# Kernel tuning notes

Measured on AMD Instinct MI355X. Metric: run time of the kernel, lower is better.

## Reference

```python
import jax, jax.numpy as jnp
import numpy as np

N = 1024                      # FFT length (init kwarg)
NF = N // 2 + 1               # rfft output length = len(freq)
PB_LO = 40.0 / 60.0           # pulse_band[0] in Hz
PB_HI = 180.0 / 60.0          # pulse_band[1] in Hz
DELTA_HZ = 6.0 / 60.0         # self.delta after /60
W0, W1 = 1.0, 1.0             # weights[0], weights[1]
B, T = 32768, 1024


def setup_inputs() -> dict:
    key = jax.random.key(0)
    k1, k2 = jax.random.split(key)
    preds = jax.random.normal(k1, (B, T), dtype=jnp.float32)
    # realistic camera frame rates ~25-35 Hz (must exceed 2*pulse_band[1]=6 Hz)
    Fs = 25.0 + 10.0 * jax.random.uniform(k2, (B,), dtype=jnp.float32)
    return {"preds": preds, "Fs": Fs}


def reference(preds, Fs):
    idx = jnp.arange(NF)                                            # [Nf]
    # freq = linspace(0, Fs/2, Nf) per sample -> [B, Nf]
    freq = (Fs[:, None] * 0.5) * (idx.astype(jnp.float32) / (NF - 1))
    left = jnp.argmin(jnp.abs(freq - PB_LO), axis=1)                # [B] int
    right = jnp.argmin(jnp.abs(freq - PB_HI), axis=1)               # [B] int

    psd = jnp.abs(jnp.fft.rfft(preds, n=N)) ** 2                    # [B, Nf]
    total = jnp.sum(psd, axis=-1)                                   # [B]

    l = left[:, None]
    r = right[:, None]
    out_band = (idx < l) | (idx >= r)                               # psd[:left] + psd[right:]
    band_loss = jnp.sum(jnp.where(out_band, psd, 0.0), axis=-1) / (1e-8 + total)

    in_band = (idx >= l) & (idx < r)
    # argmax(psd[left:right]) + left  (psd >= 0, so -inf mask is safe)
    peak = jnp.argmax(jnp.where(in_band, psd, -jnp.inf), axis=1)    # [B]
    # delta = max(1, round(self.delta / (Fs/2/len(freq))))  (round half-to-even, as Python)
    delta = jnp.maximum(1.0, jnp.round(DELTA_HZ / (Fs * 0.5 / NF))).astype(jnp.int32)

    p = peak[:, None]
    d = delta[:, None]
    # psd[left:peak-delta] + psd[peak+delta:right]  (empty slices -> 0 via mask)
    sparse_mask = in_band & ((idx < p - d) | (idx >= p + d))
    num = jnp.sum(jnp.where(sparse_mask, psd, 0.0), axis=-1)
    # sum(psd[left:right] + 1e-8) adds 1e-8 per in-band bin, keep faithful
    den = jnp.sum(jnp.where(in_band, psd + 1e-8, 0.0), axis=-1)
    sparse_loss = num / den

    return W0 * jnp.mean(band_loss) + W1 * jnp.mean(sparse_loss)
```

## Files before the change

kernel.cpp:

```cpp
#include <hip/hip_runtime.h>
#include <cmath>

#define BATCH 32768
#define SROW 66

struct cplx { float x, y; };
__device__ __forceinline__ cplx cadd(cplx a, cplx b){ return {a.x+b.x, a.y+b.y}; }
__device__ __forceinline__ cplx csub(cplx a, cplx b){ return {a.x-b.x, a.y-b.y}; }
__device__ __forceinline__ cplx cmul(cplx a, cplx b){ return {a.x*b.x - a.y*b.y, a.x*b.y + a.y*b.x}; }
__device__ __forceinline__ cplx cmul_mi(cplx a){ return {a.y, -a.x}; }
__device__ __forceinline__ cplx cmul_w81(cplx a){ const float c=0.70710678f; return {c*(a.x+a.y), c*(a.y-a.x)}; }
__device__ __forceinline__ cplx cmul_w83(cplx a){ const float c=0.70710678f; return {c*(a.y-a.x), -c*(a.x+a.y)}; }

__device__ __forceinline__ void dft8(cplx a[8]) {
    cplx t0=cadd(a[0],a[4]), t4=csub(a[0],a[4]);
    cplx t1=cadd(a[1],a[5]), t5=csub(a[1],a[5]);
    cplx t2=cadd(a[2],a[6]), t6=csub(a[2],a[6]);
    cplx t3=cadd(a[3],a[7]), t7=csub(a[3],a[7]);
    cplx u0=cadd(t0,t2), u2=csub(t0,t2);
    cplx u1=cadd(t1,t3), u3=cmul_mi(csub(t1,t3));
    a[0]=cadd(u0,u1); a[4]=csub(u0,u1); a[2]=cadd(u2,u3); a[6]=csub(u2,u3);
    cplx v0=t4, v1=cmul_w81(t5), v2=cmul_mi(t6), v3=cmul_w83(t7);
    cplx w0=cadd(v0,v2), w2=csub(v0,v2);
    cplx w1=cadd(v1,v3), w3=cmul_mi(csub(v1,v3));
    a[1]=cadd(w0,w1); a[5]=csub(w0,w1); a[3]=cadd(w2,w3); a[7]=csub(w2,w3);
}

__device__ __forceinline__ int nearest_bin(float fs, float target) {
    float x = target * 1024.0f / fs;
    int i0 = (int)floorf(x);
    int lo = max(0, i0 - 1), hi = min(512, i0 + 2);
    int bi = lo; float bd = 1e30f;
    for (int i = lo; i <= hi; ++i) {
        float fr = (fs * 0.5f) * ((float)i / 512.0f);
        float d = fabsf(fr - target);
        if (d < bd) { bd = d; bi = i; }
    }
    return bi;
}

__global__ __launch_bounds__(256) void fft_loss_kernel(
    const float* __restrict__ preds, const float* __restrict__ Fs,
    float* __restrict__ blockpartial)
{
    __shared__ float2 lds[4][8 * SROW];
    __shared__ float sblk[4];

    const int tid  = threadIdx.x;
    const int wv   = tid >> 6;
    const int lane = tid & 63;
    const int row  = blockIdx.x * 4 + wv;

    float2* sm = lds[wv];
    const float2* x2 = reinterpret_cast<const float2*>(preds) + (size_t)row * 512;

    cplx z[8];
#pragma unroll
    for (int n1 = 0; n1 < 8; ++n1) {
        float2 v = x2[n1 * 64 + lane];
        z[n1] = {v.x, v.y};
    }
    dft8(z);
    {
        float sb, cb;
        __sincosf(-0.012271846f * (float)lane, &sb, &cb);
        cplx w = {cb, sb}, u = w;
#pragma unroll
        for (int r = 1; r < 8; ++r) { z[r] = cmul(z[r], u); u = cmul(u, w); }
    }
#pragma unroll
    for (int r = 0; r < 8; ++r) sm[r * SROW + lane] = make_float2(z[r].x, z[r].y);

    const int rB = lane & 7, m0 = lane >> 3;
    cplx b[8];
#pragma unroll
    for (int m1 = 0; m1 < 8; ++m1) {
        float2 v = sm[rB * SROW + 8 * m1 + m0];
        b[m1] = {v.x, v.y};
    }
    dft8(b);
    {
        float sb, cb;
        __sincosf(-0.09817477f * (float)m0, &sb, &cb);
        cplx w = {cb, sb}, u = w;
#pragma unroll
        for (int s = 1; s < 8; ++s) { b[s] = cmul(b[s], u); u = cmul(u, w); }
    }
#pragma unroll
    for (int s = 0; s < 8; ++s) {
        sm[rB * SROW + 8 * m0 + ((s + m0) & 7)] = make_float2(b[s].x, b[s].y);
    }

    const int sC = lane >> 3;
    cplx c[8];
#pragma unroll
    for (int m = 0; m < 8; ++m) {
        float2 v = sm[rB * SROW + 8 * m + ((sC + m) & 7)];
        c[m] = {v.x, v.y};
    }
    dft8(c);

    const float fs  = Fs[row];
    const int left  = nearest_bin(fs, (float)(40.0 / 60.0));
    const int right = nearest_bin(fs, 3.0f);
    const int pl    = (64 - lane) & 63;

    float psd[8];
    float total = 0.f, inb = 0.f, best = -1.f;
    int besti = 1 << 30;
    float sk, ck;
    __sincosf(-0.0061359233f * (float)lane, &sk, &ck);
    cplx wk = {ck, sk};
    const cplx wstep = {0.92387953f, -0.38268343f};
#pragma unroll
    for (int t = 0; t < 8; ++t) {
        cplx a = c[t];
        float px = __shfl(c[7 - t].x, pl);
        float py = __shfl(c[7 - t].y, pl);
        if (lane == 0) { px = c[(8 - t) & 7].x; py = c[(8 - t) & 7].y; }
        float ex = 0.5f * (a.x + px), ey = 0.5f * (a.y - py);
        float dx = a.x - px,          dy = a.y + py;
        float ox = 0.5f * dy,         oy = -0.5f * dx;
        float Xr = ex + wk.x * ox - wk.y * oy;
        float Xi = ey + wk.x * oy + wk.y * ox;
        float v  = Xr * Xr + Xi * Xi;
        psd[t] = v;
        total += v;
        int k = lane + 64 * t;
        if (k >= left && k < right) {
            inb += v;
            if (v > best) { best = v; besti = k; }
        }
        wk = cmul(wk, wstep);
    }
    if (lane == 0) {
        float d = c[0].x - c[0].y;
        total += d * d;
    }

#pragma unroll
    for (int off = 32; off > 0; off >>= 1) {
        total += __shfl_down(total, off);
        inb   += __shfl_down(inb, off);
        float ob = __shfl_down(best, off);
        int   oi = __shfl_down(besti, off);
        if (ob > best || (ob == best && oi < besti)) { best = ob; besti = oi; }
    }
    const int bbi = __shfl(besti, 0);
    int delta = (int)rintf(0.1f / ((fs * 0.5f) / 513.0f));
    if (delta < 1) delta = 1;
    const int lo = max(left, bbi - delta), hi = min(right, bbi + delta);
    float wsum = 0.f;
#pragma unroll
    for (int t = 0; t < 8; ++t) {
        int k = lane + 64 * t;
        if (k >= lo && k < hi) wsum += psd[t];
    }
#pragma unroll
    for (int off = 32; off > 0; off >>= 1) wsum += __shfl_down(wsum, off);

    if (lane == 0) {
        float band = (total - inb) / (1e-8f + total);
        float den  = inb + 1e-8f * (float)(right - left);
        sblk[wv] = band + (inb - wsum) / den;
    }
    __syncthreads();
    if (tid == 0) blockpartial[blockIdx.x] = sblk[0] + sblk[1] + sblk[2] + sblk[3];
}

__global__ __launch_bounds__(1024) void reduce_kernel(
    const float* __restrict__ bp, float* __restrict__ out)
{
    __shared__ float w[16];
    const int t = threadIdx.x;
    float acc = 0.f;
#pragma unroll
    for (int i = 0; i < 8; ++i) acc += bp[t + 1024 * i];
    for (int off = 32; off > 0; off >>= 1) acc += __shfl_down(acc, off);
    const int lane = t & 63, wvi = t >> 6;
    if (lane == 0) w[wvi] = acc;
    __syncthreads();
    if (t == 0) {
        float s = 0.f;
        for (int i = 0; i < 16; ++i) s += w[i];
        out[0] = s * (1.0f / (float)BATCH);
    }
}

extern "C" void kernel_launch(void* const* d_in, const int* in_sizes, int n_in,
                              void* d_out, int out_size, void* d_ws, size_t ws_size,
                              hipStream_t stream) {
    const float* preds = (const float*)d_in[0];
    const float* Fs    = (const float*)d_in[1];
    float* bp          = (float*)d_ws;
    float* out         = (float*)d_out;

    fft_loss_kernel<<<BATCH / 4, 256, 0, stream>>>(preds, Fs, bp);
    reduce_kernel<<<1, 1024, 0, stream>>>(bp, out);
}
```

Baseline: 194.5 us.

## Process two rows per wave with vectorized complex math and DPP reductions

```diff
diff --git a/kernel.cpp b/kernel.cpp
--- a/kernel.cpp
+++ b/kernel.cpp
@@ -2,28 +2,50 @@
 #include <cmath>
 
 #define BATCH 32768
-#define SROW 66
-
-struct cplx { float x, y; };
-__device__ __forceinline__ cplx cadd(cplx a, cplx b){ return {a.x+b.x, a.y+b.y}; }
-__device__ __forceinline__ cplx csub(cplx a, cplx b){ return {a.x-b.x, a.y-b.y}; }
-__device__ __forceinline__ cplx cmul(cplx a, cplx b){ return {a.x*b.x - a.y*b.y, a.x*b.y + a.y*b.x}; }
-__device__ __forceinline__ cplx cmul_mi(cplx a){ return {a.y, -a.x}; }
-__device__ __forceinline__ cplx cmul_w81(cplx a){ const float c=0.70710678f; return {c*(a.x+a.y), c*(a.y-a.x)}; }
-__device__ __forceinline__ cplx cmul_w83(cplx a){ const float c=0.70710678f; return {c*(a.y-a.x), -c*(a.x+a.y)}; }
-
-__device__ __forceinline__ void dft8(cplx a[8]) {
-    cplx t0=cadd(a[0],a[4]), t4=csub(a[0],a[4]);
-    cplx t1=cadd(a[1],a[5]), t5=csub(a[1],a[5]);
-    cplx t2=cadd(a[2],a[6]), t6=csub(a[2],a[6]);
-    cplx t3=cadd(a[3],a[7]), t7=csub(a[3],a[7]);
-    cplx u0=cadd(t0,t2), u2=csub(t0,t2);
-    cplx u1=cadd(t1,t3), u3=cmul_mi(csub(t1,t3));
-    a[0]=cadd(u0,u1); a[4]=csub(u0,u1); a[2]=cadd(u2,u3); a[6]=csub(u2,u3);
-    cplx v0=t4, v1=cmul_w81(t5), v2=cmul_mi(t6), v3=cmul_w83(t7);
-    cplx w0=cadd(v0,v2), w2=csub(v0,v2);
-    cplx w1=cadd(v1,v3), w3=cmul_mi(csub(v1,v3));
-    a[1]=cadd(w0,w1); a[5]=csub(w0,w1); a[3]=cadd(w2,w3); a[7]=csub(w2,w3);
+#define SROW  66
+
+typedef float v2f __attribute__((ext_vector_type(2)));
+
+__device__ __forceinline__ v2f mkc(float r, float i) { v2f t; t.x = r; t.y = i; return t; }
+__device__ __forceinline__ v2f cmul(v2f a, v2f b) {
+    v2f s = mkc(-a.y, a.x);
+    return a * b.x + s * b.y;
+}
+__device__ __forceinline__ v2f cmul_mi(v2f a){ return mkc(a.y, -a.x); }
+__device__ __forceinline__ v2f cmul_w81(v2f a){ const float C=0.70710678f; return mkc(C*(a.x+a.y), C*(a.y-a.x)); }
+__device__ __forceinline__ v2f cmul_w83(v2f a){ const float C=0.70710678f; return mkc(C*(a.y-a.x), -C*(a.x+a.y)); }
+
+__device__ __forceinline__ void dft8(v2f a[8]) {
+    v2f t0=a[0]+a[4], t4=a[0]-a[4];
+    v2f t1=a[1]+a[5], t5=a[1]-a[5];
+    v2f t2=a[2]+a[6], t6=a[2]-a[6];
+    v2f t3=a[3]+a[7], t7=a[3]-a[7];
+    v2f u0=t0+t2, u2=t0-t2;
+    v2f u1=t1+t3, u3=cmul_mi(t1-t3);
+    a[0]=u0+u1; a[4]=u0-u1; a[2]=u2+u3; a[6]=u2-u3;
+    v2f v0=t4, v1=cmul_w81(t5), v2=cmul_mi(t6), v3=cmul_w83(t7);
+    v2f w0=v0+v2, w2=v0-v2;
+    v2f w1=v1+v3, w3=cmul_mi(v1-v3);
+    a[1]=w0+w1; a[5]=w0-w1; a[3]=w2+w3; a[7]=w2-w3;
+}
+
+__device__ __forceinline__ float wave_sum64(float x) {
+    x += __int_as_float(__builtin_amdgcn_update_dpp(0, __float_as_int(x), 0x111, 0xf, 0xf, true));
+    x += __int_as_float(__builtin_amdgcn_update_dpp(0, __float_as_int(x), 0x112, 0xf, 0xf, true));
+    x += __int_as_float(__builtin_amdgcn_update_dpp(0, __float_as_int(x), 0x114, 0xf, 0xf, true));
+    x += __int_as_float(__builtin_amdgcn_update_dpp(0, __float_as_int(x), 0x118, 0xf, 0xf, true));
+    x += __int_as_float(__builtin_amdgcn_update_dpp(0, __float_as_int(x), 0x142, 0xf, 0xf, true));
+    x += __int_as_float(__builtin_amdgcn_update_dpp(0, __float_as_int(x), 0x143, 0xf, 0xf, true));
+    return __int_as_float(__builtin_amdgcn_readlane(__float_as_int(x), 63));
+}
+__device__ __forceinline__ int wave_argmax64(float best, int besti) {
+#define AM_STEP(ctrl) { \
+    float ob = __int_as_float(__builtin_amdgcn_update_dpp(__float_as_int(best), __float_as_int(best), ctrl, 0xf, 0xf, false)); \
+    int   oi = __builtin_amdgcn_update_dpp(besti, besti, ctrl, 0xf, 0xf, false); \
+    if (ob > best || (ob == best && oi < besti)) { best = ob; besti = oi; } }
+    AM_STEP(0x111) AM_STEP(0x112) AM_STEP(0x114) AM_STEP(0x118) AM_STEP(0x142) AM_STEP(0x143)
+#undef AM_STEP
+    return __builtin_amdgcn_readlane(besti, 63);
 }
 
 __device__ __forceinline__ int nearest_bin(float fs, float target) {
@@ -39,144 +61,152 @@
     return bi;
 }
 
-__global__ __launch_bounds__(256) void fft_loss_kernel(
+__global__ __launch_bounds__(128, 4) void fft_loss_kernel(
     const float* __restrict__ preds, const float* __restrict__ Fs,
-    float* __restrict__ blockpartial)
+    float* __restrict__ wavepartial)
 {
-    __shared__ float2 lds[4][8 * SROW];
-    __shared__ float sblk[4];
+    __shared__ v2f lds[2][2][8 * SROW];
 
     const int tid  = threadIdx.x;
     const int wv   = tid >> 6;
     const int lane = tid & 63;
-    const int row  = blockIdx.x * 4 + wv;
-
-    float2* sm = lds[wv];
-    const float2* x2 = reinterpret_cast<const float2*>(preds) + (size_t)row * 512;
-
-    cplx z[8];
-#pragma unroll
-    for (int n1 = 0; n1 < 8; ++n1) {
-        float2 v = x2[n1 * 64 + lane];
-        z[n1] = {v.x, v.y};
-    }
-    dft8(z);
+    const int row0 = blockIdx.x * 4 + wv * 2;
+
+    v2f (*sm)[8 * SROW] = lds[wv];
+    const v2f* x2 = reinterpret_cast<const v2f*>(preds) + (size_t)row0 * 512;
+
+    v2f z[2][8];
+#pragma unroll
+    for (int rr = 0; rr < 2; ++rr)
+#pragma unroll
+        for (int n1 = 0; n1 < 8; ++n1)
+            z[rr][n1] = x2[rr * 512 + n1 * 64 + lane];
+
     {
         float sb, cb;
         __sincosf(-0.012271846f * (float)lane, &sb, &cb);
-        cplx w = {cb, sb}, u = w;
-#pragma unroll
-        for (int r = 1; r < 8; ++r) { z[r] = cmul(z[r], u); u = cmul(u, w); }
-    }
-#pragma unroll
-    for (int r = 0; r < 8; ++r) sm[r * SROW + lane] = make_float2(z[r].x, z[r].y);
+        v2f w1 = mkc(cb, sb);
+        v2f w2 = cmul(w1, w1), w3 = cmul(w2, w1), w4 = cmul(w2, w2);
+        v2f w5 = cmul(w3, w2), w6 = cmul(w3, w3), w7 = cmul(w4, w3);
+#pragma unroll
+        for (int rr = 0; rr < 2; ++rr) {
+            dft8(z[rr]);
+            z[rr][1]=cmul(z[rr][1],w1); z[rr][2]=cmul(z[rr][2],w2); z[rr][3]=cmul(z[rr][3],w3);
+            z[rr][4]=cmul(z[rr][4],w4); z[rr][5]=cmul(z[rr][5],w5); z[rr][6]=cmul(z[rr][6],w6);
+            z[rr][7]=cmul(z[rr][7],w7);
+#pragma unroll
+            for (int r = 0; r < 8; ++r) sm[rr][r * SROW + lane] = z[rr][r];
+        }
+    }
 
     const int rB = lane & 7, m0 = lane >> 3;
-    cplx b[8];
-#pragma unroll
-    for (int m1 = 0; m1 < 8; ++m1) {
-        float2 v = sm[rB * SROW + 8 * m1 + m0];
-        b[m1] = {v.x, v.y};
-    }
-    dft8(b);
     {
         float sb, cb;
         __sincosf(-0.09817477f * (float)m0, &sb, &cb);
-        cplx w = {cb, sb}, u = w;
-#pragma unroll
-        for (int s = 1; s < 8; ++s) { b[s] = cmul(b[s], u); u = cmul(u, w); }
-    }
-#pragma unroll
-    for (int s = 0; s < 8; ++s) {
-        sm[rB * SROW + 8 * m0 + ((s + m0) & 7)] = make_float2(b[s].x, b[s].y);
+        v2f b1 = mkc(cb, sb);
+        v2f b2 = cmul(b1, b1), b3 = cmul(b2, b1), b4 = cmul(b2, b2);
+        v2f b5 = cmul(b3, b2), b6 = cmul(b3, b3), b7 = cmul(b4, b3);
+#pragma unroll
+        for (int rr = 0; rr < 2; ++rr) {
+#pragma unroll
+            for (int m1 = 0; m1 < 8; ++m1) z[rr][m1] = sm[rr][rB * SROW + 8 * m1 + m0];
+            dft8(z[rr]);
+            z[rr][1]=cmul(z[rr][1],b1); z[rr][2]=cmul(z[rr][2],b2); z[rr][3]=cmul(z[rr][3],b3);
+            z[rr][4]=cmul(z[rr][4],b4); z[rr][5]=cmul(z[rr][5],b5); z[rr][6]=cmul(z[rr][6],b6);
+            z[rr][7]=cmul(z[rr][7],b7);
+#pragma unroll
+            for (int s = 0; s < 8; ++s)
+                sm[rr][rB * SROW + 8 * m0 + ((s + m0) & 7)] = z[rr][s];
+        }
     }
 
     const int sC = lane >> 3;
-    cplx c[8];
-#pragma unroll
-    for (int m = 0; m < 8; ++m) {
-        float2 v = sm[rB * SROW + 8 * m + ((sC + m) & 7)];
-        c[m] = {v.x, v.y};
-    }
-    dft8(c);
-
-    const float fs  = Fs[row];
-    const int left  = nearest_bin(fs, (float)(40.0 / 60.0));
-    const int right = nearest_bin(fs, 3.0f);
-    const int pl    = (64 - lane) & 63;
-
-    float psd[8];
-    float total = 0.f, inb = 0.f, best = -1.f;
-    int besti = 1 << 30;
-    float sk, ck;
-    __sincosf(-0.0061359233f * (float)lane, &sk, &ck);
-    cplx wk = {ck, sk};
-    const cplx wstep = {0.92387953f, -0.38268343f};
-#pragma unroll
-    for (int t = 0; t < 8; ++t) {
-        cplx a = c[t];
-        float px = __shfl(c[7 - t].x, pl);
-        float py = __shfl(c[7 - t].y, pl);
-        if (lane == 0) { px = c[(8 - t) & 7].x; py = c[(8 - t) & 7].y; }
-        float ex = 0.5f * (a.x + px), ey = 0.5f * (a.y - py);
-        float dx = a.x - px,          dy = a.y + py;
-        float ox = 0.5f * dy,         oy = -0.5f * dx;
-        float Xr = ex + wk.x * ox - wk.y * oy;
-        float Xi = ey + wk.x * oy + wk.y * ox;
-        float v  = Xr * Xr + Xi * Xi;
-        psd[t] = v;
-        total += v;
-        int k = lane + 64 * t;
-        if (k >= left && k < right) {
-            inb += v;
-            if (v > best) { best = v; besti = k; }
-        }
-        wk = cmul(wk, wstep);
-    }
-    if (lane == 0) {
-        float d = c[0].x - c[0].y;
-        total += d * d;
-    }
-
-#pragma unroll
-    for (int off = 32; off > 0; off >>= 1) {
-        total += __shfl_down(total, off);
-        inb   += __shfl_down(inb, off);
-        float ob = __shfl_down(best, off);
-        int   oi = __shfl_down(besti, off);
-        if (ob > best || (ob == best && oi < besti)) { best = ob; besti = oi; }
-    }
-    const int bbi = __shfl(besti, 0);
-    int delta = (int)rintf(0.1f / ((fs * 0.5f) / 513.0f));
-    if (delta < 1) delta = 1;
-    const int lo = max(left, bbi - delta), hi = min(right, bbi + delta);
-    float wsum = 0.f;
-#pragma unroll
-    for (int t = 0; t < 8; ++t) {
-        int k = lane + 64 * t;
-        if (k >= lo && k < hi) wsum += psd[t];
-    }
-#pragma unroll
-    for (int off = 32; off > 0; off >>= 1) wsum += __shfl_down(wsum, off);
-
-    if (lane == 0) {
+#pragma unroll
+    for (int rr = 0; rr < 2; ++rr) {
+#pragma unroll
+        for (int m = 0; m < 8; ++m) z[rr][m] = sm[rr][rB * SROW + 8 * m + ((sC + m) & 7)];
+        dft8(z[rr]);
+    }
+
+    const float fs_[2] = {Fs[row0], Fs[row0 + 1]};
+    const int pl = (64 - lane) & 63;
+
+    float wk0x, wk0y;
+    {
+        float sk, ck;
+        __sincosf(-0.0061359233f * (float)lane, &sk, &ck);
+        wk0x = ck; wk0y = sk;
+    }
+    const float WC[8] = {1.f, 0.92387953f, 0.70710678f, 0.38268343f, 0.f, -0.38268343f, -0.70710678f, -0.92387953f};
+    const float WS[8] = {0.f, -0.38268343f, -0.70710678f, -0.92387953f, -1.f, -0.92387953f, -0.70710678f, -0.38268343f};
+
+    float acc = 0.f;
+    float psd[2][8];
+#pragma unroll
+    for (int rr = 0; rr < 2; ++rr) {
+        const int left  = nearest_bin(fs_[rr], (float)(40.0 / 60.0));
+        const int right = nearest_bin(fs_[rr], 3.0f);
+        float total = 0.f, inb = 0.f, best = -1.f;
+        int besti = 1 << 30;
+#pragma unroll
+        for (int t = 0; t < 8; ++t) {
+            v2f a = z[rr][t];
+            float px = __shfl(z[rr][7 - t].x, pl);
+            float py = __shfl(z[rr][7 - t].y, pl);
+            if (lane == 0) { px = z[rr][(8 - t) & 7].x; py = z[rr][(8 - t) & 7].y; }
+            float wkx = wk0x * WC[t] - wk0y * WS[t];
+            float wky = wk0x * WS[t] + wk0y * WC[t];
+            float ex = 0.5f * (a.x + px), ey = 0.5f * (a.y - py);
+            float dx = a.x - px,          dy = a.y + py;
+            float ox = 0.5f * dy,         oy = -0.5f * dx;
+            float Xr = ex + wkx * ox - wky * oy;
+            float Xi = ey + wkx * oy + wky * ox;
+            float v  = Xr * Xr + Xi * Xi;
+            psd[rr][t] = v;
+            total += v;
+            int k = lane + 64 * t;
+            if (k >= left && k < right) {
+                inb += v;
+                if (v > best) { best = v; besti = k; }
+            }
+        }
+        if (lane == 0) {
+            float d = z[rr][0].x - z[rr][0].y;
+            total += d * d;
+        }
+
+        total = wave_sum64(total);
+        inb   = wave_sum64(inb);
+        const int bbi = wave_argmax64(best, besti);
+
+        int delta = (int)rintf(0.1f / ((fs_[rr] * 0.5f) / 513.0f));
+        if (delta < 1) delta = 1;
+        const int lo = max(left, bbi - delta), hi = min(right, bbi + delta);
+        float wsum = 0.f;
+#pragma unroll
+        for (int t = 0; t < 8; ++t) {
+            int k = lane + 64 * t;
+            if (k >= lo && k < hi) wsum += psd[rr][t];
+        }
+        wsum = wave_sum64(wsum);
+
         float band = (total - inb) / (1e-8f + total);
         float den  = inb + 1e-8f * (float)(right - left);
-        sblk[wv] = band + (inb - wsum) / den;
-    }
-    __syncthreads();
-    if (tid == 0) blockpartial[blockIdx.x] = sblk[0] + sblk[1] + sblk[2] + sblk[3];
+        acc += band + (inb - wsum) / den;
+    }
+
+    if (lane == 0) wavepartial[blockIdx.x * 2 + wv] = acc;
 }
 
 __global__ __launch_bounds__(1024) void reduce_kernel(
-    const float* __restrict__ bp, float* __restrict__ out)
+    const float* __restrict__ wp, float* __restrict__ out)
 {
     __shared__ float w[16];
     const int t = threadIdx.x;
     float acc = 0.f;
 #pragma unroll
-    for (int i = 0; i < 8; ++i) acc += bp[t + 1024 * i];
-    for (int off = 32; off > 0; off >>= 1) acc += __shfl_down(acc, off);
+    for (int i = 0; i < 16; ++i) acc += wp[t + 1024 * i];
+    acc = wave_sum64(acc);
     const int lane = t & 63, wvi = t >> 6;
     if (lane == 0) w[wvi] = acc;
     __syncthreads();
@@ -192,9 +222,9 @@
                               hipStream_t stream) {
     const float* preds = (const float*)d_in[0];
     const float* Fs    = (const float*)d_in[1];
-    float* bp          = (float*)d_ws;
+    float* wp          = (float*)d_ws;
     float* out         = (float*)d_out;
 
-    fft_loss_kernel<<<BATCH / 4, 256, 0, stream>>>(preds, Fs, bp);
-    reduce_kernel<<<1, 1024, 0, stream>>>(bp, out);
-}
+    fft_loss_kernel<<<BATCH / 4, 128, 0, stream>>>(preds, Fs, wp);
+    reduce_kernel<<<1, 1024, 0, stream>>>(wp, out);
+}
```

New measurement: 193.7 us. No clear change (-0.4%).
